# Kernel optimization log

Hardware: AMD Instinct MI355X
Metric: run time of the kernel (lower is better)

Reference implementation:

```python
import jax, jax.numpy as jnp
import numpy as np

DIM, NH, NKV, HD = 4096, 32, 8, 128
B, KV_LEN, WINDOW = 32, 4096, 4096
G = NH // NKV  # q heads per kv head (GQA group)


def setup_inputs() -> dict:
    key = jax.random.key(0)
    ks = jax.random.split(key, 7)
    s = 1.0 / np.sqrt(DIM)
    return {
        "x": jax.random.normal(ks[0], (1, 1, B, DIM), jnp.float32),
        "wqkv": jax.random.normal(ks[1], (DIM, DIM + 2 * NKV * HD), jnp.float32) * s,
        "wo": jax.random.normal(ks[2], (DIM, DIM), jnp.float32) * s,
        "rot_mat": jax.random.normal(ks[3], (HD, HD), jnp.float32) * (1.0 / np.sqrt(HD)),
        "cache_k": jax.random.normal(ks[4], (B, NKV, KV_LEN, HD), jnp.float32),
        "cache_v": jax.random.normal(ks[5], (B, NKV, KV_LEN, HD), jnp.float32),
        "attn_mask": jnp.zeros((1, NH, B, WINDOW), jnp.float32),
        "current_pos": 4095,
    }


def reference(x, wqkv, wo, rot_mat, cache_k, cache_v, attn_mask, current_pos):
    # fused QKV projection: (1,1,B,DIM) @ (DIM,6144) -> (1,1,B,6144)
    xqkv = x @ wqkv
    q = xqkv[..., : NH * HD].reshape(1, 1, B, NH, HD)
    k = xqkv[..., NH * HD : (NH + NKV) * HD].reshape(1, 1, B, NKV, HD)
    v = xqkv[..., (NH + NKV) * HD :].reshape(1, 1, B, NKV, HD)
    # nlp_create_qkv_heads layout: (seq, n_heads, batch, head_dim)
    q = jnp.transpose(q[:, 0], (0, 2, 1, 3))  # (1, NH, B, HD)
    k = jnp.transpose(k[:, 0], (0, 2, 1, 3))  # (1, NKV, B, HD)
    v = jnp.transpose(v[:, 0], (0, 2, 1, 3))  # (1, NKV, B, HD)
    # RoPE as matmul on last dim
    q = q @ rot_mat
    k = k @ rot_mat
    # KV-cache update at current_pos: cache is (B, NKV, KV_LEN, HD)
    cache_k = cache_k.at[:, :, current_pos, :].set(jnp.transpose(k[0], (1, 0, 2)))
    cache_v = cache_v.at[:, :, current_pos, :].set(jnp.transpose(v[0], (1, 0, 2)))
    # unpad valid region (padded to nearest 32, capped by sliding window)
    L = min(((current_pos + 1 + 31) // 32) * 32, WINDOW)
    keys = cache_k[:, :, :L]    # (B, NKV, L, HD)
    values = cache_v[:, :, :L]  # (B, NKV, L, HD)
    # grouped attention: q (1, NKV, G, B, HD) vs keys (B, NKV, L, HD)
    qg = q.reshape(1, NKV, G, B, HD)
    scores = jnp.einsum("qkgbd,bkld->qkgbl", qg, keys)  # (1,NKV,G,B,L)
    scores = scores.reshape(1, NH, B, L) / jnp.sqrt(jnp.float32(HD))
    scores = scores + attn_mask[..., :L]
    probs = jax.nn.softmax(scores, axis=-1)
    out = jnp.einsum("qkgbl,bkld->qkgbd", probs.reshape(1, NKV, G, B, L), values)
    out = out.reshape(1, NH, B, HD)
    # concatenate heads -> (1,1,B,DIM)
    out = jnp.transpose(out, (0, 2, 1, 3)).reshape(1, 1, B, NH * HD)
    return out @ wo
```

## Files before the change

### kernel.cpp

```cpp
#include <hip/hip_runtime.h>
#include <hip/hip_bf16.h>

#define BB 32
#define DIM 4096
#define NH 32
#define NKV 8
#define HD 128
#define KVLEN 4096
#define QKVC 6144
#define GQ 4

__global__ __launch_bounds__(256) void k_qkv(const float* __restrict__ x,
                                             const float* __restrict__ w,
                                             float* __restrict__ xqkv) {
    int j  = blockIdx.x * 256 + threadIdx.x;
    int d0 = blockIdx.y * 256;
    float acc[BB];
#pragma unroll
    for (int b = 0; b < BB; ++b) acc[b] = 0.f;
    for (int dd = d0; dd < d0 + 256; dd += 4) {
        float w0 = w[(size_t)(dd + 0) * QKVC + j];
        float w1 = w[(size_t)(dd + 1) * QKVC + j];
        float w2 = w[(size_t)(dd + 2) * QKVC + j];
        float w3 = w[(size_t)(dd + 3) * QKVC + j];
#pragma unroll
        for (int b = 0; b < BB; ++b) {
            float4 xv = *(const float4*)&x[b * DIM + dd];
            acc[b] = fmaf(xv.x, w0, fmaf(xv.y, w1, fmaf(xv.z, w2, fmaf(xv.w, w3, acc[b]))));
        }
    }
#pragma unroll
    for (int b = 0; b < BB; ++b) atomicAdd(&xqkv[(size_t)b * QKVC + j], acc[b]);
}

__global__ __launch_bounds__(128) void k_rot(const float* __restrict__ xqkv,
                                             const float* __restrict__ rot,
                                             const int* __restrict__ curpos,
                                             float* __restrict__ qws,
                                             float* __restrict__ ck,
                                             float* __restrict__ cv) {
    int c  = blockIdx.x;
    int b  = blockIdx.y;
    int dp = threadIdx.x;
    int pos = *curpos;
    const float* row = &xqkv[(size_t)b * QKVC + c * HD];
    if (c < 40) {
        float acc = 0.f;
#pragma unroll 4
        for (int d = 0; d < HD; ++d) acc = fmaf(row[d], rot[d * HD + dp], acc);
        if (c < 32) {
            qws[((size_t)b * NH + c) * HD + dp] = acc;
        } else {
            int kvh = c - 32;
            ck[(((size_t)b * NKV + kvh) * KVLEN + pos) * HD + dp] = acc;
        }
    } else {
        int kvh = c - 40;
        cv[(((size_t)b * NKV + kvh) * KVLEN + pos) * HD + dp] = row[dp];
    }
}

__global__ __launch_bounds__(256) void k_qk(const float* __restrict__ ck,
                                            const float* __restrict__ qws,
                                            const float* __restrict__ mask,
                                            const int* __restrict__ curpos,
                                            float* __restrict__ scores,
                                            float2* __restrict__ stats) {
    __shared__ float Kl[64 * 132];
    __shared__ float ql[4 * 128];
    int bkv = blockIdx.x;
    int split = blockIdx.y;
    int b = bkv >> 3, kv = bkv & 7;
    int tid = threadIdx.x;
    int g = tid >> 6, lane = tid & 63;
    int pos = *curpos;
    int L = min((((pos + 1) + 31) >> 5) << 5, KVLEN);

    for (int i = tid; i < GQ * HD; i += 256)
        ql[i] = qws[((size_t)b * NH + kv * GQ) * HD + i];
    __syncthreads();

    const float scale = 0.08838834764831845f;
    float m = -3.0e38f, lsum = 0.f;
    int l0 = split * 1024;
    int h = kv * GQ + g;

    for (int t = 0; t < 16; ++t) {
        const float4* Kg = (const float4*)&ck[((size_t)bkv * KVLEN + l0 + t * 64) * HD];
#pragma unroll
        for (int i = 0; i < 8; ++i) {
            int c4i = i * 256 + tid;
            int row = c4i >> 5, c4 = c4i & 31;
            *(float4*)&Kl[row * 132 + c4 * 4] = Kg[row * 32 + c4];
        }
        __syncthreads();
        float s = 0.f;
#pragma unroll
        for (int d4 = 0; d4 < 32; ++d4) {
            float4 kk = *(const float4*)&Kl[lane * 132 + d4 * 4];
            float4 qq = *(const float4*)&ql[g * HD + d4 * 4];
            s += kk.x * qq.x + kk.y * qq.y + kk.z * qq.z + kk.w * qq.w;
        }
        int l = l0 + t * 64 + lane;
        s = s * scale + mask[((size_t)h * BB + b) * KVLEN + l];
        if (l >= L) {
            s = -3.0e38f;
        } else {
            if (s > m) { lsum = lsum * __expf(m - s) + 1.f; m = s; }
            else       { lsum += __expf(s - m); }
        }
        scores[((size_t)(bkv * GQ + g)) * KVLEN + l] = s;
        __syncthreads();
    }
#pragma unroll
    for (int off = 32; off > 0; off >>= 1) {
        float mo = __shfl_xor(m, off);
        float lo = __shfl_xor(lsum, off);
        float M2 = fmaxf(m, mo);
        lsum = lsum * __expf(m - M2) + lo * __expf(mo - M2);
        m = M2;
    }
    if (lane == 0) stats[(bkv * GQ + g) * 4 + split] = make_float2(m, lsum);
}

__global__ void k_stats(const float2* __restrict__ stats, float2* __restrict__ mfin) {
    int i = blockIdx.x * 256 + threadIdx.x;
    if (i >= BB * NKV * GQ) return;
    float m = -3.0e38f, l = 0.f;
#pragma unroll
    for (int s = 0; s < 4; ++s) {
        float2 p = stats[i * 4 + s];
        float M2 = fmaxf(m, p.x);
        l = l * __expf(m - M2) + p.y * __expf(p.x - M2);
        m = M2;
    }
    mfin[i] = make_float2(m, l > 0.f ? 1.f / l : 0.f);
}

__global__ __launch_bounds__(512) void k_pv(const float* __restrict__ cv,
                                            const float* __restrict__ scores,
                                            const float2* __restrict__ mfin,
                                            float* __restrict__ attn) {
    __shared__ float p_lds[4][GQ][512];
    __shared__ float o_lds[4][GQ][HD];
    int bkv = blockIdx.x;
    int tid = threadIdx.x;
    int sub = tid >> 7, d = tid & 127;
    float acc[GQ] = {0.f, 0.f, 0.f, 0.f};
    float2 ML[GQ];
#pragma unroll
    for (int g = 0; g < GQ; ++g) ML[g] = mfin[bkv * GQ + g];

    for (int half = 0; half < 2; ++half) {
        int l0 = sub * 1024 + half * 512;
#pragma unroll
        for (int i = 0; i < 16; ++i) {
            int flat = i * 128 + (tid & 127);
            int g = flat >> 9, l = flat & 511;
            float s = scores[((size_t)(bkv * GQ + g)) * KVLEN + l0 + l];
            p_lds[sub][g][l] = __expf(s - ML[g].x) * ML[g].y;
        }
        __syncthreads();
        const float* Vg = &cv[((size_t)bkv * KVLEN + l0) * HD];
#pragma unroll 4
        for (int l = 0; l < 512; ++l) {
            float v = Vg[(size_t)l * HD + d];
#pragma unroll
            for (int g = 0; g < GQ; ++g) acc[g] = fmaf(p_lds[sub][g][l], v, acc[g]);
        }
        __syncthreads();
    }
#pragma unroll
    for (int g = 0; g < GQ; ++g) o_lds[sub][g][d] = acc[g];
    __syncthreads();
    {
        int g = tid >> 7, d2 = tid & 127;
        float o = o_lds[0][g][d2] + o_lds[1][g][d2] + o_lds[2][g][d2] + o_lds[3][g][d2];
        int b = bkv >> 3, kv = bkv & 7;
        attn[(size_t)b * DIM + (kv * GQ + g) * HD + d2] = o;
    }
}

__global__ __launch_bounds__(256) void k_wo(const float* __restrict__ attn,
                                            const float* __restrict__ wo,
                                            float* __restrict__ out) {
    int j  = blockIdx.x * 256 + threadIdx.x;
    int d0 = blockIdx.y * 256;
    float acc[BB];
#pragma unroll
    for (int b = 0; b < BB; ++b) acc[b] = 0.f;
    for (int dd = d0; dd < d0 + 256; dd += 4) {
        float w0 = wo[(size_t)(dd + 0) * DIM + j];
        float w1 = wo[(size_t)(dd + 1) * DIM + j];
        float w2 = wo[(size_t)(dd + 2) * DIM + j];
        float w3 = wo[(size_t)(dd + 3) * DIM + j];
#pragma unroll
        for (int b = 0; b < BB; ++b) {
            float4 av = *(const float4*)&attn[b * DIM + dd];
            acc[b] = fmaf(av.x, w0, fmaf(av.y, w1, fmaf(av.z, w2, fmaf(av.w, w3, acc[b]))));
        }
    }
#pragma unroll
    for (int b = 0; b < BB; ++b) atomicAdd(&out[(size_t)b * DIM + j], acc[b]);
}

extern "C" void kernel_launch(void* const* d_in, const int* in_sizes, int n_in,
                              void* d_out, int out_size, void* d_ws, size_t ws_size,
                              hipStream_t stream) {
    const float* x    = (const float*)d_in[0];
    const float* wqkv = (const float*)d_in[1];
    const float* wo   = (const float*)d_in[2];
    const float* rot  = (const float*)d_in[3];
    float* ck         = (float*)d_in[4];
    float* cv         = (float*)d_in[5];
    const float* mask = (const float*)d_in[6];
    const int* curpos = (const int*)d_in[7];
    float* out        = (float*)d_out;

    char* ws = (char*)d_ws;
    float*  xqkv   = (float*)(ws);
    float*  qws    = (float*)(ws + 786432);
    float*  scores = (float*)(ws + 1310720);
    float2* stats  = (float2*)(ws + 18087936);
    float2* mfin   = (float2*)(ws + 18120704);
    float*  attn   = (float*)(ws + 18128896);

    hipMemsetAsync(xqkv, 0, 786432, stream);
    hipMemsetAsync(out, 0, (size_t)out_size * sizeof(float), stream);

    k_qkv <<<dim3(QKVC / 256, 16), 256, 0, stream>>>(x, wqkv, xqkv);
    k_rot <<<dim3(48, BB),        128, 0, stream>>>(xqkv, rot, curpos, qws, ck, cv);
    k_qk  <<<dim3(BB * NKV, 4),   256, 0, stream>>>(ck, qws, mask, curpos, scores, stats);
    k_stats<<<dim3(4),            256, 0, stream>>>(stats, mfin);
    k_pv  <<<dim3(BB * NKV),      512, 0, stream>>>(cv, scores, mfin, attn);
    k_wo  <<<dim3(DIM / 256, 16), 256, 0, stream>>>(attn, wo, out);
}
```

Before: 1.375 ms.

## Split GEMMs into more partials with reduction kernels, prefetch K, split PV

```diff
diff --git a/kernel.cpp b/kernel.cpp
--- a/kernel.cpp
+++ b/kernel.cpp
@@ -1,5 +1,4 @@
 #include <hip/hip_runtime.h>
-#include <hip/hip_bf16.h>
 
 #define BB 32
 #define DIM 4096
@@ -9,28 +8,50 @@
 #define KVLEN 4096
 #define QKVC 6144
 #define GQ 4
-
-__global__ __launch_bounds__(256) void k_qkv(const float* __restrict__ x,
-                                             const float* __restrict__ w,
-                                             float* __restrict__ xqkv) {
+#define QKV_SPLITS 32
+#define WO_SPLITS 32
+
+__global__ __launch_bounds__(256, 4) void k_qkv(const float* __restrict__ x,
+                                                const float* __restrict__ w,
+                                                float* __restrict__ part) {
     int j  = blockIdx.x * 256 + threadIdx.x;
-    int d0 = blockIdx.y * 256;
+    int d0 = blockIdx.y * (DIM / QKV_SPLITS);
     float acc[BB];
 #pragma unroll
     for (int b = 0; b < BB; ++b) acc[b] = 0.f;
-    for (int dd = d0; dd < d0 + 256; dd += 4) {
-        float w0 = w[(size_t)(dd + 0) * QKVC + j];
-        float w1 = w[(size_t)(dd + 1) * QKVC + j];
-        float w2 = w[(size_t)(dd + 2) * QKVC + j];
-        float w3 = w[(size_t)(dd + 3) * QKVC + j];
+    for (int dd = d0; dd < d0 + DIM / QKV_SPLITS; dd += 8) {
+        float wr[8];
+#pragma unroll
+        for (int k = 0; k < 8; ++k) wr[k] = w[(size_t)(dd + k) * QKVC + j];
 #pragma unroll
         for (int b = 0; b < BB; ++b) {
-            float4 xv = *(const float4*)&x[b * DIM + dd];
-            acc[b] = fmaf(xv.x, w0, fmaf(xv.y, w1, fmaf(xv.z, w2, fmaf(xv.w, w3, acc[b]))));
-        }
-    }
-#pragma unroll
-    for (int b = 0; b < BB; ++b) atomicAdd(&xqkv[(size_t)b * QKVC + j], acc[b]);
+            float4 xa = *(const float4*)&x[b * DIM + dd];
+            float4 xb = *(const float4*)&x[b * DIM + dd + 4];
+            float t = acc[b];
+            t = fmaf(xa.x, wr[0], t); t = fmaf(xa.y, wr[1], t);
+            t = fmaf(xa.z, wr[2], t); t = fmaf(xa.w, wr[3], t);
+            t = fmaf(xb.x, wr[4], t); t = fmaf(xb.y, wr[5], t);
+            t = fmaf(xb.z, wr[6], t); t = fmaf(xb.w, wr[7], t);
+            acc[b] = t;
+        }
+    }
+#pragma unroll
+    for (int b = 0; b < BB; ++b)
+        part[(size_t)blockIdx.y * (BB * QKVC) + (size_t)b * QKVC + j] = acc[b];
+}
+
+__global__ __launch_bounds__(256) void k_red(const float* __restrict__ src,
+                                             float* __restrict__ dst,
+                                             int parts, int n4) {
+    int i = blockIdx.x * 256 + threadIdx.x;
+    if (i >= n4) return;
+    const float4* s4 = (const float4*)src;
+    float4 a = s4[i];
+    for (int p = 1; p < parts; ++p) {
+        float4 b = s4[(size_t)p * n4 + i];
+        a.x += b.x; a.y += b.y; a.z += b.z; a.w += b.w;
+    }
+    ((float4*)dst)[i] = a;
 }
 
 __global__ __launch_bounds__(128) void k_rot(const float* __restrict__ xqkv,
@@ -60,12 +81,12 @@
     }
 }
 
-__global__ __launch_bounds__(256) void k_qk(const float* __restrict__ ck,
-                                            const float* __restrict__ qws,
-                                            const float* __restrict__ mask,
-                                            const int* __restrict__ curpos,
-                                            float* __restrict__ scores,
-                                            float2* __restrict__ stats) {
+__global__ __launch_bounds__(256, 4) void k_qk(const float* __restrict__ ck,
+                                               const float* __restrict__ qws,
+                                               const float* __restrict__ mask,
+                                               const int* __restrict__ curpos,
+                                               float* __restrict__ scores,
+                                               float2* __restrict__ stats) {
     __shared__ float Kl[64 * 132];
     __shared__ float ql[4 * 128];
     int bkv = blockIdx.x;
@@ -78,22 +99,30 @@
 
     for (int i = tid; i < GQ * HD; i += 256)
         ql[i] = qws[((size_t)b * NH + kv * GQ) * HD + i];
-    __syncthreads();
 
     const float scale = 0.08838834764831845f;
     float m = -3.0e38f, lsum = 0.f;
     int l0 = split * 1024;
     int h = kv * GQ + g;
 
+    const float4* Kbase = (const float4*)&ck[((size_t)bkv * KVLEN + l0) * HD];
+    float4 kreg[8];
+#pragma unroll
+    for (int i = 0; i < 8; ++i) kreg[i] = Kbase[i * 256 + tid];
+
     for (int t = 0; t < 16; ++t) {
-        const float4* Kg = (const float4*)&ck[((size_t)bkv * KVLEN + l0 + t * 64) * HD];
 #pragma unroll
         for (int i = 0; i < 8; ++i) {
             int c4i = i * 256 + tid;
             int row = c4i >> 5, c4 = c4i & 31;
-            *(float4*)&Kl[row * 132 + c4 * 4] = Kg[row * 32 + c4];
+            *(float4*)&Kl[row * 132 + c4 * 4] = kreg[i];
         }
         __syncthreads();
+        if (t < 15) {
+            const float4* Kn = Kbase + (size_t)(t + 1) * 2048;
+#pragma unroll
+            for (int i = 0; i < 8; ++i) kreg[i] = Kn[i * 256 + tid];
+        }
         float s = 0.f;
 #pragma unroll
         for (int d4 = 0; d4 < 32; ++d4) {
@@ -137,71 +166,83 @@
     mfin[i] = make_float2(m, l > 0.f ? 1.f / l : 0.f);
 }
 
-__global__ __launch_bounds__(512) void k_pv(const float* __restrict__ cv,
-                                            const float* __restrict__ scores,
-                                            const float2* __restrict__ mfin,
-                                            float* __restrict__ attn) {
-    __shared__ float p_lds[4][GQ][512];
-    __shared__ float o_lds[4][GQ][HD];
+__global__ __launch_bounds__(512, 6) void k_pv(const float* __restrict__ cv,
+                                               const float* __restrict__ scores,
+                                               const float2* __restrict__ mfin,
+                                               float* __restrict__ attn_part) {
     int bkv = blockIdx.x;
+    int split = blockIdx.y;
     int tid = threadIdx.x;
-    int sub = tid >> 7, d = tid & 127;
-    float acc[GQ] = {0.f, 0.f, 0.f, 0.f};
+    int d4 = tid & 31;
+    int lg = tid >> 5;
+    int l0 = split * 1024 + lg * 64;
+
     float2 ML[GQ];
 #pragma unroll
     for (int g = 0; g < GQ; ++g) ML[g] = mfin[bkv * GQ + g];
 
-    for (int half = 0; half < 2; ++half) {
-        int l0 = sub * 1024 + half * 512;
-#pragma unroll
-        for (int i = 0; i < 16; ++i) {
-            int flat = i * 128 + (tid & 127);
-            int g = flat >> 9, l = flat & 511;
-            float s = scores[((size_t)(bkv * GQ + g)) * KVLEN + l0 + l];
-            p_lds[sub][g][l] = __expf(s - ML[g].x) * ML[g].y;
-        }
-        __syncthreads();
-        const float* Vg = &cv[((size_t)bkv * KVLEN + l0) * HD];
+    float4 acc[GQ];
+#pragma unroll
+    for (int g = 0; g < GQ; ++g) acc[g] = make_float4(0.f, 0.f, 0.f, 0.f);
+
+    const float* Vg = &cv[((size_t)bkv * KVLEN + l0) * HD + d4 * 4];
+    const float* Sg = &scores[(size_t)bkv * GQ * KVLEN + l0];
+
 #pragma unroll 4
-        for (int l = 0; l < 512; ++l) {
-            float v = Vg[(size_t)l * HD + d];
-#pragma unroll
-            for (int g = 0; g < GQ; ++g) acc[g] = fmaf(p_lds[sub][g][l], v, acc[g]);
-        }
-        __syncthreads();
-    }
-#pragma unroll
-    for (int g = 0; g < GQ; ++g) o_lds[sub][g][d] = acc[g];
+    for (int i = 0; i < 64; ++i) {
+        float4 v = *(const float4*)&Vg[(size_t)i * HD];
+#pragma unroll
+        for (int g = 0; g < GQ; ++g) {
+            float s = Sg[(size_t)g * KVLEN + i];
+            float p = __expf(s - ML[g].x) * ML[g].y;
+            acc[g].x = fmaf(p, v.x, acc[g].x);
+            acc[g].y = fmaf(p, v.y, acc[g].y);
+            acc[g].z = fmaf(p, v.z, acc[g].z);
+            acc[g].w = fmaf(p, v.w, acc[g].w);
+        }
+    }
+
+    __shared__ float red[16][GQ][HD];
+#pragma unroll
+    for (int g = 0; g < GQ; ++g) *(float4*)&red[lg][g][d4 * 4] = acc[g];
     __syncthreads();
     {
-        int g = tid >> 7, d2 = tid & 127;
-        float o = o_lds[0][g][d2] + o_lds[1][g][d2] + o_lds[2][g][d2] + o_lds[3][g][d2];
+        int g2 = tid >> 7, d = tid & 127;
+        float o = 0.f;
+#pragma unroll
+        for (int k = 0; k < 16; ++k) o += red[k][g2][d];
         int b = bkv >> 3, kv = bkv & 7;
-        attn[(size_t)b * DIM + (kv * GQ + g) * HD + d2] = o;
-    }
-}
-
-__global__ __launch_bounds__(256) void k_wo(const float* __restrict__ attn,
-                                            const float* __restrict__ wo,
-                                            float* __restrict__ out) {
+        attn_part[(size_t)split * (BB * DIM) + (size_t)b * DIM + (kv * GQ + g2) * HD + d] = o;
+    }
+}
+
+__global__ __launch_bounds__(256, 4) void k_wo(const float* __restrict__ attn,
+                                               const float* __restrict__ wo,
+                                               float* __restrict__ part) {
     int j  = blockIdx.x * 256 + threadIdx.x;
-    int d0 = blockIdx.y * 256;
+    int d0 = blockIdx.y * (DIM / WO_SPLITS);
     float acc[BB];
 #pragma unroll
     for (int b = 0; b < BB; ++b) acc[b] = 0.f;
-    for (int dd = d0; dd < d0 + 256; dd += 4) {
-        float w0 = wo[(size_t)(dd + 0) * DIM + j];
-        float w1 = wo[(size_t)(dd + 1) * DIM + j];
-        float w2 = wo[(size_t)(dd + 2) * DIM + j];
-        float w3 = wo[(size_t)(dd + 3) * DIM + j];
+    for (int dd = d0; dd < d0 + DIM / WO_SPLITS; dd += 8) {
+        float wr[8];
+#pragma unroll
+        for (int k = 0; k < 8; ++k) wr[k] = wo[(size_t)(dd + k) * DIM + j];
 #pragma unroll
         for (int b = 0; b < BB; ++b) {
-            float4 av = *(const float4*)&attn[b * DIM + dd];
-            acc[b] = fmaf(av.x, w0, fmaf(av.y, w1, fmaf(av.z, w2, fmaf(av.w, w3, acc[b]))));
-        }
-    }
-#pragma unroll
-    for (int b = 0; b < BB; ++b) atomicAdd(&out[(size_t)b * DIM + j], acc[b]);
+            float4 xa = *(const float4*)&attn[b * DIM + dd];
+            float4 xb = *(const float4*)&attn[b * DIM + dd + 4];
+            float t = acc[b];
+            t = fmaf(xa.x, wr[0], t); t = fmaf(xa.y, wr[1], t);
+            t = fmaf(xa.z, wr[2], t); t = fmaf(xa.w, wr[3], t);
+            t = fmaf(xb.x, wr[4], t); t = fmaf(xb.y, wr[5], t);
+            t = fmaf(xb.z, wr[6], t); t = fmaf(xb.w, wr[7], t);
+            acc[b] = t;
+        }
+    }
+#pragma unroll
+    for (int b = 0; b < BB; ++b)
+        part[(size_t)blockIdx.y * (BB * DIM) + (size_t)b * DIM + j] = acc[b];
 }
 
 extern "C" void kernel_launch(void* const* d_in, const int* in_sizes, int n_in,
@@ -218,20 +259,23 @@
     float* out        = (float*)d_out;
 
     char* ws = (char*)d_ws;
-    float*  xqkv   = (float*)(ws);
-    float*  qws    = (float*)(ws + 786432);
-    float*  scores = (float*)(ws + 1310720);
-    float2* stats  = (float2*)(ws + 18087936);
-    float2* mfin   = (float2*)(ws + 18120704);
-    float*  attn   = (float*)(ws + 18128896);
-
-    hipMemsetAsync(xqkv, 0, 786432, stream);
-    hipMemsetAsync(out, 0, (size_t)out_size * sizeof(float), stream);
-
-    k_qkv <<<dim3(QKVC / 256, 16), 256, 0, stream>>>(x, wqkv, xqkv);
-    k_rot <<<dim3(48, BB),        128, 0, stream>>>(xqkv, rot, curpos, qws, ck, cv);
-    k_qk  <<<dim3(BB * NKV, 4),   256, 0, stream>>>(ck, qws, mask, curpos, scores, stats);
-    k_stats<<<dim3(4),            256, 0, stream>>>(stats, mfin);
-    k_pv  <<<dim3(BB * NKV),      512, 0, stream>>>(cv, scores, mfin, attn);
-    k_wo  <<<dim3(DIM / 256, 16), 256, 0, stream>>>(attn, wo, out);
-}
+    float*  xqkv_part = (float*)(ws);
+    float*  xqkv      = (float*)(ws + 25165824);
+    float*  qws       = (float*)(ws + 25952256);
+    float*  scores    = (float*)(ws + 26476544);
+    float2* stats     = (float2*)(ws + 43253760);
+    float2* mfin      = (float2*)(ws + 43286528);
+    float*  attn_part = (float*)(ws + 43294720);
+    float*  attn      = (float*)(ws + 45391872);
+    float*  out_part  = (float*)(ws + 45916160);
+
+    k_qkv  <<<dim3(QKVC / 256, QKV_SPLITS), 256, 0, stream>>>(x, wqkv, xqkv_part);
+    k_red  <<<dim3(192),                    256, 0, stream>>>(xqkv_part, xqkv, QKV_SPLITS, BB * QKVC / 4);
+    k_rot  <<<dim3(48, BB),                 128, 0, stream>>>(xqkv, rot, curpos, qws, ck, cv);
+    k_qk   <<<dim3(BB * NKV, 4),            256, 0, stream>>>(ck, qws, mask, curpos, scores, stats);
+    k_stats<<<dim3(4),                      256, 0, stream>>>(stats, mfin);
+    k_pv   <<<dim3(BB * NKV, 4),            512, 0, stream>>>(cv, scores, mfin, attn_part);
+    k_red  <<<dim3(128),                    256, 0, stream>>>(attn_part, attn, 4, BB * DIM / 4);
+    k_wo   <<<dim3(DIM / 256, WO_SPLITS),   256, 0, stream>>>(attn, wo, out_part);
+    k_red  <<<dim3(128),                    256, 0, stream>>>(out_part, out, WO_SPLITS, BB * DIM / 4);
+}
```

Measured after the change: 1.397 ms. About the same (+1.6%).
